# Performance work log

Measured on AMD Instinct MI355X. Metric: run time of the kernel, lower is better.

Reference implementation:

```python
import jax, jax.numpy as jnp
import numpy as np

NUM_EMBEDDINGS = 512
EMBEDDING_DIM = 64


def setup_inputs() -> dict:
    key = jax.random.key(0)
    k1, k2 = jax.random.split(key)
    z_e = jax.random.normal(k1, (32, EMBEDDING_DIM, 64, 64), dtype=jnp.float32)
    lim = 1.0 / NUM_EMBEDDINGS
    codebook = jax.random.uniform(k2, (NUM_EMBEDDINGS, EMBEDDING_DIM),
                                  dtype=jnp.float32, minval=-lim, maxval=lim)
    return {"z_e": z_e, "codebook": codebook}


def reference(z_e, codebook):
    B, C, H, W = z_e.shape
    # [B,C,H,W] -> [N, C] with N = B*H*W (channels-last flatten)
    z_flat = jnp.transpose(z_e, (0, 2, 3, 1)).reshape(-1, C)
    # squared L2 distance via ||a||^2 + ||b||^2 - 2 a.b (same math, no NxKxC tensor)
    d = (jnp.sum(z_flat * z_flat, axis=1, keepdims=True)          # [N,1]
         + jnp.sum(codebook * codebook, axis=1)[None, :]           # [1,K]
         - 2.0 * jnp.einsum('nc,kc->nk', z_flat, codebook))        # [N,K]
    encoding_indices = jnp.argmin(d, axis=1)                       # [N] int
    z_q = codebook[encoding_indices].reshape(B, H, W, C)
    z_q = jnp.transpose(z_q, (0, 3, 1, 2))                         # [B,C,H,W]
    return z_q, encoding_indices
```

## Files before the change

kernel.cpp:

```cpp
#include <hip/hip_runtime.h>
#include <stdint.h>


#pragma clang fp contract(off)

#define KCODES 512
#define CDIM 64
#define HW 4096
#define ZQ_ELEMS 8388608

typedef float f2 __attribute__((ext_vector_type(2)));

static __device__ __forceinline__ f2 pk_fma_s(f2 a, uint64_t b, f2 c) {
    f2 d;
    asm("v_pk_fma_f32 %0, %1, %2, %3" : "=v"(d) : "v"(a), "s"(b), "v"(c));
    return d;
}
static __device__ __forceinline__ f2 pk_add(f2 a, f2 b) {
    f2 d;
    asm("v_pk_add_f32 %0, %1, %2" : "=v"(d) : "v"(a), "v"(b));
    return d;
}

__global__ __launch_bounds__(256, 4) void vq_kernel(
    const float* __restrict__ z_e,
    const float* __restrict__ cb,
    float* __restrict__ out)
{
    __shared__ float cnorm[KCODES];
    __shared__ float dcand[4 * 64];
    __shared__ int   kcand[4 * 64];

    for (int k = (int)threadIdx.x; k < KCODES; k += 256) {
        const float* row = cb + k * CDIM;
        float r[8];
        #pragma unroll
        for (int j = 0; j < 8; ++j) r[j] = row[j] * row[j];
        #pragma unroll
        for (int i = 8; i < 64; i += 8) {
            #pragma unroll
            for (int j = 0; j < 8; ++j) r[j] = r[j] + row[i + j] * row[i + j];
        }
        cnorm[k] = ((r[0] + r[1]) + (r[2] + r[3])) + ((r[4] + r[5]) + (r[6] + r[7]));
    }

    const int lane = (int)threadIdx.x & 63;
    const int g = __builtin_amdgcn_readfirstlane((int)threadIdx.x >> 6);
    const int n0 = (int)blockIdx.x * 64;
    const int b = n0 / HW;
    const int hw0 = n0 % HW;
    const float* zp = z_e + (size_t)b * CDIM * HW + hw0 + lane;

    f2 zz2[CDIM / 2];
    #pragma unroll
    for (int m = 0; m < CDIM / 2; ++m) {
        f2 t;
        t.x = zp[(size_t)(2 * m) * HW];
        t.y = zp[(size_t)(2 * m + 1) * HW];
        zz2[m] = t;
    }

    float sz;
    {
        f2 pr[4];
        #pragma unroll
        for (int t = 0; t < 4; ++t) pr[t] = zz2[t] * zz2[t];
        #pragma unroll
        for (int i = 8; i < 64; i += 8) {
            #pragma unroll
            for (int t = 0; t < 4; ++t) {
                f2 zt = zz2[(i + 2 * t) / 2];
                pr[t] = pr[t] + zt * zt;
            }
        }
        float s01 = pr[0].x + pr[0].y;
        float s23 = pr[1].x + pr[1].y;
        float s45 = pr[2].x + pr[2].y;
        float s67 = pr[3].x + pr[3].y;
        sz = (s01 + s23) + (s45 + s67);
    }

    __syncthreads();

    f2 zero; zero.x = 0.f; zero.y = 0.f;

    float best = 3.4e38f;
    int bk = 0;
    const int k0 = g * 128;

    for (int i = 0; i < 128; ++i) {
        const int k = k0 + i;
        const float* ck = cb + k * CDIM;
        const uint64_t* cq = (const uint64_t*)(const void*)ck;

        f2 pv[8];
        #pragma unroll
        for (int j = 0; j < 8; ++j) {
            pv[j] = pk_fma_s(zz2[j], cq[j],
                      pk_fma_s(zz2[8 + j], cq[8 + j],
                        pk_fma_s(zz2[16 + j], cq[16 + j],
                          pk_fma_s(zz2[24 + j], cq[24 + j], zero))));
        }
        f2 pe0 = pk_add(pv[0], pv[4]), pe1 = pk_add(pv[1], pv[5]);
        f2 pe2 = pk_add(pv[2], pv[6]), pe3 = pk_add(pv[3], pv[7]);
        f2 pf0 = pk_add(pe0, pe2), pf1 = pk_add(pe1, pe3);
        f2 pt = pk_add(pf0, pf1);
        float dot = pt.x + pt.y;

        float A = sz + cnorm[k];
        float d = fmaf(dot, -2.f, A);

        if (d < best) { best = d; bk = k; }
    }

    dcand[g * 64 + lane] = best;
    kcand[g * 64 + lane] = bk;
    __syncthreads();

    float bd = dcand[lane];
    int bi = kcand[lane];
    #pragma unroll
    for (int gg = 1; gg < 4; ++gg) {
        float d2 = dcand[gg * 64 + lane];
        int   k2 = kcand[gg * 64 + lane];
        if (d2 < bd) { bd = d2; bi = k2; }
    }

    if (g == 0) out[ZQ_ELEMS + n0 + lane] = (float)bi;

    const float* row = cb + (size_t)bi * CDIM;
    float* op = out + (size_t)b * CDIM * HW + hw0 + lane;
    #pragma unroll
    for (int c = 0; c < 16; ++c) {
        const int ch = g * 16 + c;
        op[(size_t)ch * HW] = row[ch];
    }
}

extern "C" void kernel_launch(void* const* d_in, const int* in_sizes, int n_in,
                              void* d_out, int out_size, void* d_ws, size_t ws_size,
                              hipStream_t stream) {
    const float* z_e = (const float*)d_in[0];
    const float* cb  = (const float*)d_in[1];
    float* out = (float*)d_out;
    vq_kernel<<<dim3(2048), dim3(256), 0, stream>>>(z_e, cb, out);
}
```

Baseline: 196.3 us.

## Stage codebook tiles in LDS and give each wave its own pixels

Moves codebook-norm computation into a separate small kernel writing to workspace. The main kernel now assigns 64 distinct pixels per wave, with each thread scanning all 512 codes instead of splitting codes across waves. It also stages 128-code tiles of the codebook into shared memory per phase and reads operands from LDS rather than as scalar loads. This removes the cross-wave argmin reduction and the redundant per-block norm computation, but it adds an extra launch, LDS traffic per FMA and fewer blocks (512) with reduced occupancy.

```diff
diff --git a/kernel.cpp b/kernel.cpp
--- a/kernel.cpp
+++ b/kernel.cpp
@@ -11,9 +11,9 @@
 
 typedef float f2 __attribute__((ext_vector_type(2)));
 
-static __device__ __forceinline__ f2 pk_fma_s(f2 a, uint64_t b, f2 c) {
+static __device__ __forceinline__ f2 pk_fma(f2 a, f2 b, f2 c) {
     f2 d;
-    asm("v_pk_fma_f32 %0, %1, %2, %3" : "=v"(d) : "v"(a), "s"(b), "v"(c));
+    asm("v_pk_fma_f32 %0, %1, %2, %3" : "=v"(d) : "v"(a), "v"(b), "v"(c));
     return d;
 }
 static __device__ __forceinline__ f2 pk_add(f2 a, f2 b) {
@@ -22,31 +22,37 @@
     return d;
 }
 
-__global__ __launch_bounds__(256, 4) void vq_kernel(
+__global__ __launch_bounds__(256) void vq_norms(const float* __restrict__ cb,
+                                                float* __restrict__ cnorm_g)
+{
+    const int k = (int)blockIdx.x * 256 + (int)threadIdx.x;
+    if (k >= KCODES) return;
+    const float* row = cb + k * CDIM;
+    float r[8];
+    #pragma unroll
+    for (int j = 0; j < 8; ++j) r[j] = row[j] * row[j];
+    #pragma unroll
+    for (int i = 8; i < 64; i += 8) {
+        #pragma unroll
+        for (int j = 0; j < 8; ++j) r[j] = r[j] + row[i + j] * row[i + j];
+    }
+    cnorm_g[k] = ((r[0] + r[1]) + (r[2] + r[3])) + ((r[4] + r[5]) + (r[6] + r[7]));
+}
+
+__global__ __launch_bounds__(256, 2) void vq_main(
     const float* __restrict__ z_e,
     const float* __restrict__ cb,
+    const float* __restrict__ cnorm_g,
     float* __restrict__ out)
 {
-    __shared__ float cnorm[KCODES];
-    __shared__ float dcand[4 * 64];
-    __shared__ int   kcand[4 * 64];
+    __shared__ float rows[128 * CDIM];
+    __shared__ float cnorm_s[128];
 
-    for (int k = (int)threadIdx.x; k < KCODES; k += 256) {
-        const float* row = cb + k * CDIM;
-        float r[8];
-        #pragma unroll
-        for (int j = 0; j < 8; ++j) r[j] = row[j] * row[j];
-        #pragma unroll
-        for (int i = 8; i < 64; i += 8) {
-            #pragma unroll
-            for (int j = 0; j < 8; ++j) r[j] = r[j] + row[i + j] * row[i + j];
-        }
-        cnorm[k] = ((r[0] + r[1]) + (r[2] + r[3])) + ((r[4] + r[5]) + (r[6] + r[7]));
-    }
+    const int tid = (int)threadIdx.x;
+    const int lane = tid & 63;
+    const int w = __builtin_amdgcn_readfirstlane(tid >> 6);
 
-    const int lane = (int)threadIdx.x & 63;
-    const int g = __builtin_amdgcn_readfirstlane((int)threadIdx.x >> 6);
-    const int n0 = (int)blockIdx.x * 64;
+    const int n0 = (int)blockIdx.x * 256 + w * 64;
     const int b = n0 / HW;
     const int hw0 = n0 % HW;
     const float* zp = z_e + (size_t)b * CDIM * HW + hw0 + lane;
@@ -80,60 +86,58 @@
         sz = (s01 + s23) + (s45 + s67);
     }
 
-    __syncthreads();
-
     f2 zero; zero.x = 0.f; zero.y = 0.f;
 
     float best = 3.4e38f;
     int bk = 0;
-    const int k0 = g * 128;
 
-    for (int i = 0; i < 128; ++i) {
-        const int k = k0 + i;
-        const float* ck = cb + k * CDIM;
-        const uint64_t* cq = (const uint64_t*)(const void*)ck;
+    for (int phase = 0; phase < 4; ++phase) {
+        __syncthreads();
+        {
+            const float4* src = (const float4*)(cb + (size_t)phase * 128 * CDIM);
+            float4* dst = (float4*)rows;
+            #pragma unroll
+            for (int i = 0; i < 8; ++i) dst[tid + 256 * i] = src[tid + 256 * i];
+            if (tid < 128) cnorm_s[tid] = cnorm_g[phase * 128 + tid];
+        }
+        __syncthreads();
 
-        f2 pv[8];
-        #pragma unroll
-        for (int j = 0; j < 8; ++j) {
-            pv[j] = pk_fma_s(zz2[j], cq[j],
-                      pk_fma_s(zz2[8 + j], cq[8 + j],
-                        pk_fma_s(zz2[16 + j], cq[16 + j],
-                          pk_fma_s(zz2[24 + j], cq[24 + j], zero))));
+        for (int i = 0; i < 128; ++i) {
+            const f2* cp = (const f2*)(rows + i * CDIM);
+
+            f2 pv[8];
+            #pragma unroll
+            for (int j = 0; j < 8; ++j) {
+                f2 c0 = cp[j];
+                f2 c1 = cp[8 + j];
+                f2 c2 = cp[16 + j];
+                f2 c3 = cp[24 + j];
+                pv[j] = pk_fma(zz2[j], c0,
+                          pk_fma(zz2[8 + j], c1,
+                            pk_fma(zz2[16 + j], c2,
+                              pk_fma(zz2[24 + j], c3, zero))));
+            }
+            f2 pe0 = pk_add(pv[0], pv[4]), pe1 = pk_add(pv[1], pv[5]);
+            f2 pe2 = pk_add(pv[2], pv[6]), pe3 = pk_add(pv[3], pv[7]);
+            f2 pf0 = pk_add(pe0, pe2), pf1 = pk_add(pe1, pe3);
+            f2 pt = pk_add(pf0, pf1);
+            float dot = pt.x + pt.y;
+
+            float A = sz + cnorm_s[i];
+            float d = fmaf(dot, -2.f, A);
+
+            const int k = phase * 128 + i;
+            if (d < best) { best = d; bk = k; }
         }
-        f2 pe0 = pk_add(pv[0], pv[4]), pe1 = pk_add(pv[1], pv[5]);
-        f2 pe2 = pk_add(pv[2], pv[6]), pe3 = pk_add(pv[3], pv[7]);
-        f2 pf0 = pk_add(pe0, pe2), pf1 = pk_add(pe1, pe3);
-        f2 pt = pk_add(pf0, pf1);
-        float dot = pt.x + pt.y;
-
-        float A = sz + cnorm[k];
-        float d = fmaf(dot, -2.f, A);
-
-        if (d < best) { best = d; bk = k; }
     }
 
-    dcand[g * 64 + lane] = best;
-    kcand[g * 64 + lane] = bk;
-    __syncthreads();
+    out[ZQ_ELEMS + n0 + lane] = (float)bk;
 
-    float bd = dcand[lane];
-    int bi = kcand[lane];
-    #pragma unroll
-    for (int gg = 1; gg < 4; ++gg) {
-        float d2 = dcand[gg * 64 + lane];
-        int   k2 = kcand[gg * 64 + lane];
-        if (d2 < bd) { bd = d2; bi = k2; }
-    }
-
-    if (g == 0) out[ZQ_ELEMS + n0 + lane] = (float)bi;
-
-    const float* row = cb + (size_t)bi * CDIM;
+    const float* row = cb + (size_t)bk * CDIM;
     float* op = out + (size_t)b * CDIM * HW + hw0 + lane;
     #pragma unroll
-    for (int c = 0; c < 16; ++c) {
-        const int ch = g * 16 + c;
-        op[(size_t)ch * HW] = row[ch];
+    for (int c = 0; c < CDIM; ++c) {
+        op[(size_t)c * HW] = row[c];
     }
 }
 
@@ -143,5 +147,7 @@
     const float* z_e = (const float*)d_in[0];
     const float* cb  = (const float*)d_in[1];
     float* out = (float*)d_out;
-    vq_kernel<<<dim3(2048), dim3(256), 0, stream>>>(z_e, cb, out);
+    float* cnorm_g = (float*)d_ws;
+    vq_norms<<<dim3(2), dim3(256), 0, stream>>>(cb, cnorm_g);
+    vq_main<<<dim3(512), dim3(256), 0, stream>>>(z_e, cb, cnorm_g, out);
 }
```

Measured after the change: 354.3 us. 1.8x slower.
